# Optimization experiments

Hardware: AMD Instinct MI355X
Metric: run time of the kernel (lower is better)

The kernel has to match this reference:

```python
import jax, jax.numpy as jnp
import numpy as np

N = 50000
E = 800000
D = 128          # in_dim = hidden_dim = out_dim
H = 4            # heads
C = D // H       # per-head channels = 32
L = 3            # num_layers
SLOPE = 0.2
BN_EPS = 1e-5


def setup_inputs() -> dict:
    key = jax.random.key(0)
    ks = jax.random.split(key, 12)
    x = jax.random.normal(ks[0], (N, D), dtype=jnp.float32)
    ei = jax.random.randint(ks[1], (2, E), 0, N, dtype=jnp.int64)
    # remove accidental self loops (PyG removes then re-adds them)
    src, dst = ei[0], ei[1]
    src = jnp.where(src == dst, (src + 1) % N, src)
    edge_index = jnp.stack([src, dst])
    s = 1.0 / np.sqrt(D)
    Wl = jax.random.normal(ks[2], (L, D, D), dtype=jnp.float32) * s
    Wr = jax.random.normal(ks[3], (L, D, D), dtype=jnp.float32) * s
    att = jax.random.normal(ks[4], (L, H, C), dtype=jnp.float32) * (1.0 / np.sqrt(C))
    bias = jnp.zeros((L, D), dtype=jnp.float32)
    Wres = jax.random.normal(ks[5], (L, D, D), dtype=jnp.float32) * s
    gamma = jnp.ones((L, D), dtype=jnp.float32)
    beta = jnp.zeros((L, D), dtype=jnp.float32)
    W_out = jax.random.normal(ks[6], (D, D), dtype=jnp.float32) * s
    b_out = jnp.zeros((D,), dtype=jnp.float32)
    return {"x": x, "edge_index": edge_index, "Wl": Wl, "Wr": Wr, "att": att,
            "bias": bias, "Wres": Wres, "gamma": gamma, "beta": beta,
            "W_out": W_out, "b_out": b_out}


def _segment_softmax(scores, seg, num_segments):
    # scores: [E, H], seg: [E] dst ids
    m = jax.ops.segment_max(scores, seg, num_segments=num_segments)  # [N, H]
    ex = jnp.exp(scores - m[seg])
    denom = jax.ops.segment_sum(ex, seg, num_segments=num_segments)  # [N, H]
    return ex / denom[seg]


def _gatv2_layer(x, src, dst, Wl_, Wr_, att_, b_, Wres_):
    xl = (x @ Wl_).reshape(N, H, C)   # source-side transform
    xr = (x @ Wr_).reshape(N, H, C)   # target-side transform
    msg = xl[src]                      # [E, H, C]
    pre = jax.nn.leaky_relu(msg + xr[dst], SLOPE)
    e = jnp.einsum('ehc,hc->eh', pre, att_)          # [E, H]
    alpha = _segment_softmax(e, dst, N)              # [E, H]
    agg = jax.ops.segment_sum(alpha[..., None] * msg, dst, num_segments=N)
    return agg.reshape(N, D) + b_ + x @ Wres_


def _batch_norm(x, g, b):
    mu = jnp.mean(x, axis=0)
    var = jnp.mean(jnp.square(x - mu), axis=0)  # biased, as in torch BN
    return (x - mu) * jax.lax.rsqrt(var + BN_EPS) * g + b


def reference(x, edge_index, Wl, Wr, att, bias, Wres, gamma, beta, W_out, b_out):
    # add self loops once (same augmentation every layer)
    loops = jnp.arange(N, dtype=edge_index.dtype)
    src = jnp.concatenate([edge_index[0], loops])
    dst = jnp.concatenate([edge_index[1], loops])
    for i in range(L):
        x = _gatv2_layer(x, src, dst, Wl[i], Wr[i], att[i], bias[i], Wres[i])
        x = _batch_norm(x, gamma[i], beta[i])
        x = jax.nn.leaky_relu(x, SLOPE)
        # dropout = identity in eval
    return x @ W_out + b_out
```

## Files before the change

### kernel.cpp

```cpp
#include <hip/hip_runtime.h>
#include <hip/hip_bf16.h>

constexpr int N = 50000;
constexpr int E = 800000;
constexpr int D = 128;
constexpr int H = 4;
constexpr int C = 32;
constexpr int L = 3;
constexpr int E2 = E + N;
constexpr float SLOPE = 0.2f;
constexpr float BN_EPS = 1e-5f;
constexpr float LOG2E = 1.4426950408889634f;
constexpr int TILES = (N + 63) / 64;

typedef __attribute__((ext_vector_type(8))) short bf16x8_t;
typedef __attribute__((ext_vector_type(4))) float f32x4_t;
typedef __attribute__((ext_vector_type(2))) float v2f;

using hbf = __hip_bfloat16;

__device__ __forceinline__ float fast_exp2(float x) { return __builtin_amdgcn_exp2f(x); }

__device__ __forceinline__ short f2bf(float v) {
    hbf h = __float2bfloat16(v);
    return *reinterpret_cast<short*>(&h);
}
__device__ __forceinline__ v2f bfpair_to_v2(unsigned int u) {
    v2f r;
    r.x = __uint_as_float(u << 16);
    r.y = __uint_as_float(u & 0xffff0000u);
    return r;
}

__global__ void count_kernel(const int* __restrict__ ei, int* __restrict__ counts,
                             int* __restrict__ rank) {
    int i = blockIdx.x * blockDim.x + threadIdx.x;
    if (i >= E2) return;
    int dst = (i < E) ? ei[E + i] : (i - E);
    rank[i] = atomicAdd(&counts[dst], 1);
}

__global__ __launch_bounds__(512) void scan_block_kernel(const int* __restrict__ counts,
                                                         int* __restrict__ row_ptr,
                                                         int* __restrict__ blk_sums) {
    __shared__ int s[512];
    int t = threadIdx.x;
    int i = blockIdx.x * 512 + t;
    int v = (i < N) ? counts[i] : 0;
    s[t] = v;
    __syncthreads();
    for (int off = 1; off < 512; off <<= 1) {
        int add = (t >= off) ? s[t - off] : 0;
        __syncthreads();
        s[t] += add;
        __syncthreads();
    }
    if (i < N) row_ptr[i] = s[t] - v;
    if (t == 511) blk_sums[blockIdx.x] = s[511];
}

__global__ __launch_bounds__(128) void scan_sums_kernel(int* __restrict__ blk, int nb) {
    __shared__ int s[128];
    int t = threadIdx.x;
    int v = (t < nb) ? blk[t] : 0;
    s[t] = v;
    __syncthreads();
    for (int off = 1; off < 128; off <<= 1) {
        int add = (t >= off) ? s[t - off] : 0;
        __syncthreads();
        s[t] += add;
        __syncthreads();
    }
    if (t < nb) blk[t] = s[t] - v;
}

__global__ void scan_add_kernel(int* __restrict__ row_ptr, const int* __restrict__ blk) {
    int i = blockIdx.x * blockDim.x + threadIdx.x;
    if (i < N) row_ptr[i] += blk[i >> 9];
    if (i == 0) row_ptr[N] = E2;
}

__global__ void scatter_kernel(const int* __restrict__ ei, const int* __restrict__ row_ptr,
                               const int* __restrict__ rank, int* __restrict__ col_idx) {
    int i = blockIdx.x * blockDim.x + threadIdx.x;
    if (i >= E2) return;
    int src, dst;
    if (i < E) { src = ei[i]; dst = ei[E + i]; }
    else       { src = i - E; dst = i - E; }
    col_idx[row_ptr[dst] + rank[i]] = src;
}

__global__ __launch_bounds__(256) void pack_w_kernel(
        const float* __restrict__ Wl, const float* __restrict__ Wr,
        const float* __restrict__ Wres, const float* __restrict__ Wout,
        hbf* __restrict__ Wph) {
    int gid = blockIdx.x * 256 + threadIdx.x;
    int mat = gid >> 14;
    int d = gid & 16383;
    const float* W;
    if (mat < 3)      W = Wl + (size_t)mat * 16384;
    else if (mat < 6) W = Wr + (size_t)(mat - 3) * 16384;
    else if (mat < 9) W = Wres + (size_t)(mat - 6) * 16384;
    else              W = Wout;
    int j = d & 7, lane = (d >> 3) & 63, nb = (d >> 9) & 7, ks = d >> 12;
    int k = ks * 32 + ((lane >> 4) * 8) + j;
    int n = nb * 16 + (lane & 15);
    Wph[gid] = __float2bfloat16(W[k * D + n]);
}

__global__ __launch_bounds__(256) void gemm3_mfma_kernel(
        const float* x, const float* __restrict__ sums,
        const float* __restrict__ gamma, const float* __restrict__ beta,
        const hbf* __restrict__ Wph,
        int mL, int mR, int mS, const float* __restrict__ bias,
        hbf* __restrict__ xl, hbf* __restrict__ xr, float* y) {
    __shared__ hbf xsh[64][136];
    __shared__ hbf xsl[64][136];
    __shared__ float ssl[2][128];
    int t = threadIdx.x;
    int wave = t >> 6;
    int lane = t & 63;
    int nb0 = wave * 2;
    int row0 = blockIdx.x * 64;

    if (sums && t < 128) {
        float mean = sums[t] * (1.0f / N);
        float var = fmaxf(sums[D + t] * (1.0f / N) - mean * mean, 0.f);
        float sc = gamma[t] * rsqrtf(var + BN_EPS);
        ssl[0][t] = sc;
        ssl[1][t] = beta[t] - mean * sc;
    }

    const bf16x8_t* B = (const bf16x8_t*)Wph;
    bf16x8_t bL[4][2], bR[4][2], bS[4][2];
#pragma unroll
    for (int ks = 0; ks < 4; ++ks)
#pragma unroll
        for (int j = 0; j < 2; ++j) {
            int bo = (ks * 8 + nb0 + j) * 64 + lane;
            bL[ks][j] = B[mL * 2048 + bo];
            bR[ks][j] = B[mR * 2048 + bo];
            bS[ks][j] = B[mS * 2048 + bo];
        }
    __syncthreads();

    int cg = (t & 31) * 4;
    {
        float sc_[4] = {1.f, 1.f, 1.f, 1.f}, sh_[4] = {0.f, 0.f, 0.f, 0.f};
        if (sums) {
#pragma unroll
            for (int j = 0; j < 4; ++j) { sc_[j] = ssl[0][cg + j]; sh_[j] = ssl[1][cg + j]; }
        }
        const float4* x4 = (const float4*)(x + (size_t)row0 * D);
        for (int i = t; i < 64 * 32; i += 256) {
            int r = i >> 5;
            float4 v = make_float4(0.f, 0.f, 0.f, 0.f);
            if (row0 + r < N) {
                v = x4[i];
                if (sums) {
                    v.x = fmaf(v.x, sc_[0], sh_[0]); v.x = fmaxf(v.x, SLOPE * v.x);
                    v.y = fmaf(v.y, sc_[1], sh_[1]); v.y = fmaxf(v.y, SLOPE * v.y);
                    v.z = fmaf(v.z, sc_[2], sh_[2]); v.z = fmaxf(v.z, SLOPE * v.z);
                    v.w = fmaf(v.w, sc_[3], sh_[3]); v.w = fmaxf(v.w, SLOPE * v.w);
                }
            }
            short h0 = f2bf(v.x), h1 = f2bf(v.y), h2 = f2bf(v.z), h3 = f2bf(v.w);
            float r0 = v.x - __uint_as_float(((unsigned)(unsigned short)h0) << 16);
            float r1 = v.y - __uint_as_float(((unsigned)(unsigned short)h1) << 16);
            float r2 = v.z - __uint_as_float(((unsigned)(unsigned short)h2) << 16);
            float r3 = v.w - __uint_as_float(((unsigned)(unsigned short)h3) << 16);
            short l0 = f2bf(r0), l1 = f2bf(r1), l2 = f2bf(r2), l3 = f2bf(r3);
            uint2 hp, lp;
            hp.x = (unsigned)(unsigned short)h0 | ((unsigned)(unsigned short)h1 << 16);
            hp.y = (unsigned)(unsigned short)h2 | ((unsigned)(unsigned short)h3 << 16);
            lp.x = (unsigned)(unsigned short)l0 | ((unsigned)(unsigned short)l1 << 16);
            lp.y = (unsigned)(unsigned short)l2 | ((unsigned)(unsigned short)l3 << 16);
            *(uint2*)&xsh[r][cg] = hp;
            *(uint2*)&xsl[r][cg] = lp;
        }
    }
    __syncthreads();

    int col = lane & 15;
    int koff = (lane >> 4) * 8;
    for (int mm = 0; mm < 4; ++mm) {
        int mrow = mm * 16 + (lane & 15);
        f32x4_t aL[2], aR[2], aS[2];
#pragma unroll
        for (int j = 0; j < 2; ++j) {
            aL[j] = (f32x4_t)0.f; aR[j] = (f32x4_t)0.f; aS[j] = (f32x4_t)0.f;
        }
#pragma unroll
        for (int ks = 0; ks < 4; ++ks) {
            bf16x8_t ah = *(const bf16x8_t*)&xsh[mrow][ks * 32 + koff];
            bf16x8_t al = *(const bf16x8_t*)&xsl[mrow][ks * 32 + koff];
#pragma unroll
            for (int j = 0; j < 2; ++j) {
                aL[j] = __builtin_amdgcn_mfma_f32_16x16x32_bf16(ah, bL[ks][j], aL[j], 0, 0, 0);
                aL[j] = __builtin_amdgcn_mfma_f32_16x16x32_bf16(al, bL[ks][j], aL[j], 0, 0, 0);
                aR[j] = __builtin_amdgcn_mfma_f32_16x16x32_bf16(ah, bR[ks][j], aR[j], 0, 0, 0);
                aR[j] = __builtin_amdgcn_mfma_f32_16x16x32_bf16(al, bR[ks][j], aR[j], 0, 0, 0);
                aS[j] = __builtin_amdgcn_mfma_f32_16x16x32_bf16(ah, bS[ks][j], aS[j], 0, 0, 0);
                aS[j] = __builtin_amdgcn_mfma_f32_16x16x32_bf16(al, bS[ks][j], aS[j], 0, 0, 0);
            }
        }
        int rowq = row0 + mm * 16 + (lane >> 4) * 4;
#pragma unroll
        for (int j = 0; j < 2; ++j) {
            int n = (nb0 + j) * 16 + col;
            float bv = bias[n];
#pragma unroll
            for (int r = 0; r < 4; ++r) {
                int row = rowq + r;
                if (row < N) {
                    xl[(size_t)row * D + n] = __float2bfloat16(aL[j][r]);
                    xr[(size_t)row * D + n] = __float2bfloat16(aR[j][r]);
                    y[(size_t)row * D + n]  = aS[j][r] + bv;
                }
            }
        }
    }
}

__global__ __launch_bounds__(256) void gemm_out_mfma_kernel(
        const float* __restrict__ x, const float* __restrict__ sums,
        const float* __restrict__ gamma, const float* __restrict__ beta,
        const hbf* __restrict__ Wph, const float* __restrict__ b,
        float* __restrict__ out) {
    __shared__ hbf xsh[64][136];
    __shared__ hbf xsl[64][136];
    __shared__ float ssl[2][128];
    int t = threadIdx.x;
    int wave = t >> 6;
    int lane = t & 63;
    int nb0 = wave * 2;
    int row0 = blockIdx.x * 64;

    if (t < 128) {
        float mean = sums[t] * (1.0f / N);
        float var = fmaxf(sums[D + t] * (1.0f / N) - mean * mean, 0.f);
        float sc = gamma[t] * rsqrtf(var + BN_EPS);
        ssl[0][t] = sc;
        ssl[1][t] = beta[t] - mean * sc;
    }

    const bf16x8_t* B = (const bf16x8_t*)Wph + 9 * 2048;
    bf16x8_t bW[4][2];
#pragma unroll
    for (int ks = 0; ks < 4; ++ks)
#pragma unroll
        for (int j = 0; j < 2; ++j)
            bW[ks][j] = B[(ks * 8 + nb0 + j) * 64 + lane];
    __syncthreads();

    int cg = (t & 31) * 4;
    {
        float sc_[4], sh_[4];
#pragma unroll
        for (int j = 0; j < 4; ++j) { sc_[j] = ssl[0][cg + j]; sh_[j] = ssl[1][cg + j]; }
        const float4* x4 = (const float4*)(x + (size_t)row0 * D);
        for (int i = t; i < 64 * 32; i += 256) {
            int r = i >> 5;
            float4 v = make_float4(0.f, 0.f, 0.f, 0.f);
            if (row0 + r < N) {
                v = x4[i];
                v.x = fmaf(v.x, sc_[0], sh_[0]); v.x = fmaxf(v.x, SLOPE * v.x);
                v.y = fmaf(v.y, sc_[1], sh_[1]); v.y = fmaxf(v.y, SLOPE * v.y);
                v.z = fmaf(v.z, sc_[2], sh_[2]); v.z = fmaxf(v.z, SLOPE * v.z);
                v.w = fmaf(v.w, sc_[3], sh_[3]); v.w = fmaxf(v.w, SLOPE * v.w);
            }
            short h0 = f2bf(v.x), h1 = f2bf(v.y), h2 = f2bf(v.z), h3 = f2bf(v.w);
            float r0 = v.x - __uint_as_float(((unsigned)(unsigned short)h0) << 16);
            float r1 = v.y - __uint_as_float(((unsigned)(unsigned short)h1) << 16);
            float r2 = v.z - __uint_as_float(((unsigned)(unsigned short)h2) << 16);
            float r3 = v.w - __uint_as_float(((unsigned)(unsigned short)h3) << 16);
            short l0 = f2bf(r0), l1 = f2bf(r1), l2 = f2bf(r2), l3 = f2bf(r3);
            uint2 hp, lp;
            hp.x = (unsigned)(unsigned short)h0 | ((unsigned)(unsigned short)h1 << 16);
            hp.y = (unsigned)(unsigned short)h2 | ((unsigned)(unsigned short)h3 << 16);
            lp.x = (unsigned)(unsigned short)l0 | ((unsigned)(unsigned short)l1 << 16);
            lp.y = (unsigned)(unsigned short)l2 | ((unsigned)(unsigned short)l3 << 16);
            *(uint2*)&xsh[r][cg] = hp;
            *(uint2*)&xsl[r][cg] = lp;
        }
    }
    __syncthreads();

    int col = lane & 15;
    int koff = (lane >> 4) * 8;
    for (int mm = 0; mm < 4; ++mm) {
        int mrow = mm * 16 + (lane & 15);
        f32x4_t acc[2];
        acc[0] = (f32x4_t)0.f; acc[1] = (f32x4_t)0.f;
#pragma unroll
        for (int ks = 0; ks < 4; ++ks) {
            bf16x8_t ah = *(const bf16x8_t*)&xsh[mrow][ks * 32 + koff];
            bf16x8_t al = *(const bf16x8_t*)&xsl[mrow][ks * 32 + koff];
#pragma unroll
            for (int j = 0; j < 2; ++j) {
                acc[j] = __builtin_amdgcn_mfma_f32_16x16x32_bf16(ah, bW[ks][j], acc[j], 0, 0, 0);
                acc[j] = __builtin_amdgcn_mfma_f32_16x16x32_bf16(al, bW[ks][j], acc[j], 0, 0, 0);
            }
        }
        int rowq = row0 + mm * 16 + (lane >> 4) * 4;
#pragma unroll
        for (int j = 0; j < 2; ++j) {
            int n = (nb0 + j) * 16 + col;
            float bv = b[n];
#pragma unroll
            for (int r = 0; r < 4; ++r) {
                int row = rowq + r;
                if (row < N) out[(size_t)row * D + n] = acc[j][r] + bv;
            }
        }
    }
}

__global__ __launch_bounds__(256) void gat_kernel(
        const hbf* __restrict__ xl, const hbf* __restrict__ xr,
        float* y, const int* __restrict__ row_ptr,
        const int* __restrict__ col_idx, const float* __restrict__ att) {
    int wave = threadIdx.x >> 6;
    int lane = threadIdx.x & 63;
    int e    = (lane >> 4) & 1;
    int sub  = lane & 15;
    int v = blockIdx.x * 8 + wave * 2 + (lane >> 5);
    const uint4* xlp = (const uint4*)xl;
    const uint4* xrp = (const uint4*)xr;
    uint4 xru = xrp[(size_t)v * 16 + sub];
    v2f xr_a = bfpair_to_v2(xru.x);
    v2f xr_b = bfpair_to_v2(xru.y);
    v2f xr_c = bfpair_to_v2(xru.z);
    v2f xr_d = bfpair_to_v2(xru.w);
    const float4* attf = (const float4*)att;
    float4 a4lo = attf[sub * 2];
    float4 a4hi = attf[sub * 2 + 1];
    v2f a_a; a_a.x = a4lo.x * LOG2E; a_a.y = a4lo.y * LOG2E;
    v2f a_b; a_b.x = a4lo.z * LOG2E; a_b.y = a4lo.w * LOG2E;
    v2f a_c; a_c.x = a4hi.x * LOG2E; a_c.y = a4hi.y * LOG2E;
    v2f a_d; a_d.x = a4hi.z * LOG2E; a_d.y = a4hi.w * LOG2E;
    int beg = row_ptr[v], end = row_ptr[v + 1];
    int d = end - beg;
    int dmax = max(d, __shfl_xor(d, 32));
    float l = 0.f;
    v2f acc_a = {0.f, 0.f};
    v2f acc_b = {0.f, 0.f};
    v2f acc_c = {0.f, 0.f};
    v2f acc_d = {0.f, 0.f};

    uint4 u0[2], u1[2];
    int c0[2], c1[2];
    u0[0] = xlp[(size_t)col_idx[min(beg + 0 + e, end - 1)] * 16 + sub];
    u0[1] = xlp[(size_t)col_idx[min(beg + 2 + e, end - 1)] * 16 + sub];
    u1[0] = xlp[(size_t)col_idx[min(beg + 4 + e, end - 1)] * 16 + sub];
    u1[1] = xlp[(size_t)col_idx[min(beg + 6 + e, end - 1)] * 16 + sub];
    c0[0] = col_idx[min(beg + 8 + e, end - 1)];
    c0[1] = col_idx[min(beg + 10 + e, end - 1)];
    c1[0] = col_idx[min(beg + 12 + e, end - 1)];
    c1[1] = col_idx[min(beg + 14 + e, end - 1)];

    int off = 0;
    auto process4 = [&](uint4 (&buf)[2], int (&cid)[2]) {
        v2f xa0 = bfpair_to_v2(buf[0].x);
        v2f xb0 = bfpair_to_v2(buf[0].y);
        v2f xc0 = bfpair_to_v2(buf[0].z);
        v2f xd0 = bfpair_to_v2(buf[0].w);
        v2f xa1 = bfpair_to_v2(buf[1].x);
        v2f xb1 = bfpair_to_v2(buf[1].y);
        v2f xc1 = bfpair_to_v2(buf[1].z);
        v2f xd1 = bfpair_to_v2(buf[1].w);
        buf[0] = xlp[(size_t)cid[0] * 16 + sub];
        buf[1] = xlp[(size_t)cid[1] * 16 + sub];
        cid[0] = col_idx[min(beg + off + 16 + e, end - 1)];
        cid[1] = col_idx[min(beg + off + 18 + e, end - 1)];

        v2f pa = xa0 + xr_a, pb = xb0 + xr_b;
        v2f pc = xc0 + xr_c, pd = xd0 + xr_d;
        pa = __builtin_elementwise_max(pa, pa * SLOPE);
        pb = __builtin_elementwise_max(pb, pb * SLOPE);
        pc = __builtin_elementwise_max(pc, pc * SLOPE);
        pd = __builtin_elementwise_max(pd, pd * SLOPE);
        v2f t0 = pa * a_a;
        t0 = pb * a_b + t0;
        t0 = pc * a_c + t0;
        t0 = pd * a_d + t0;
        pa = xa1 + xr_a; pb = xb1 + xr_b;
        pc = xc1 + xr_c; pd = xd1 + xr_d;
        pa = __builtin_elementwise_max(pa, pa * SLOPE);
        pb = __builtin_elementwise_max(pb, pb * SLOPE);
        pc = __builtin_elementwise_max(pc, pc * SLOPE);
        pd = __builtin_elementwise_max(pd, pd * SLOPE);
        v2f t1 = pa * a_a;
        t1 = pb * a_b + t1;
        t1 = pc * a_c + t1;
        t1 = pd * a_d + t1;
        float s0 = t0.x + t0.y;
        float s1 = t1.x + t1.y;
        s0 += __shfl_xor(s0, 1);  s1 += __shfl_xor(s1, 1);
        s0 += __shfl_xor(s0, 2);  s1 += __shfl_xor(s1, 2);
        float w0 = fast_exp2(s0);
        float w1 = fast_exp2(s1);
        w0 = (off + e < d) ? w0 : 0.f;
        w1 = (off + 2 + e < d) ? w1 : 0.f;
        l += w0 + w1;
        acc_a = xa0 * w0 + acc_a;
        acc_b = xb0 * w0 + acc_b;
        acc_c = xc0 * w0 + acc_c;
        acc_d = xd0 * w0 + acc_d;
        acc_a = xa1 * w1 + acc_a;
        acc_b = xb1 * w1 + acc_b;
        acc_c = xc1 * w1 + acc_c;
        acc_d = xd1 * w1 + acc_d;
    };

    while (true) {
        process4(u0, c0);
        off += 4;
        if (off >= dmax) break;
        process4(u1, c1);
        off += 4;
        if (off >= dmax) break;
    }
    l += __shfl_xor(l, 16);
    acc_a.x += __shfl_xor(acc_a.x, 16); acc_a.y += __shfl_xor(acc_a.y, 16);
    acc_b.x += __shfl_xor(acc_b.x, 16); acc_b.y += __shfl_xor(acc_b.y, 16);
    acc_c.x += __shfl_xor(acc_c.x, 16); acc_c.y += __shfl_xor(acc_c.y, 16);
    acc_d.x += __shfl_xor(acc_d.x, 16); acc_d.y += __shfl_xor(acc_d.y, 16);
    if (e == 0) {
        float rl = 1.f / l;
        size_t o = (size_t)v * 32 + sub * 2;
        float4 y0 = ((const float4*)y)[o];
        float4 y1 = ((const float4*)y)[o + 1];
        y0.x = fmaf(acc_a.x, rl, y0.x);
        y0.y = fmaf(acc_a.y, rl, y0.y);
        y0.z = fmaf(acc_b.x, rl, y0.z);
        y0.w = fmaf(acc_b.y, rl, y0.w);
        y1.x = fmaf(acc_c.x, rl, y1.x);
        y1.y = fmaf(acc_c.y, rl, y1.y);
        y1.z = fmaf(acc_d.x, rl, y1.z);
        y1.w = fmaf(acc_d.y, rl, y1.w);
        ((float4*)y)[o] = y0;
        ((float4*)y)[o + 1] = y1;
    }
}

__global__ __launch_bounds__(256) void bn_stats_kernel(const float* __restrict__ y,
                                                       float* __restrict__ sums) {
    __shared__ float ls[256][4];
    __shared__ float ls2[256][4];
    int t = threadIdx.x;
    float4 s = make_float4(0.f, 0.f, 0.f, 0.f);
    float4 s2 = make_float4(0.f, 0.f, 0.f, 0.f);
    const float4* y4 = (const float4*)y;
    for (int i = blockIdx.x * 256 + t; i < N * D / 4; i += gridDim.x * 256) {
        float4 v = y4[i];
        s.x += v.x; s.y += v.y; s.z += v.z; s.w += v.w;
        s2.x = fmaf(v.x, v.x, s2.x); s2.y = fmaf(v.y, v.y, s2.y);
        s2.z = fmaf(v.z, v.z, s2.z); s2.w = fmaf(v.w, v.w, s2.w);
    }
    ls[t][0] = s.x;  ls[t][1] = s.y;  ls[t][2] = s.z;  ls[t][3] = s.w;
    ls2[t][0] = s2.x; ls2[t][1] = s2.y; ls2[t][2] = s2.z; ls2[t][3] = s2.w;
    __syncthreads();
    if (t < D) {
        int g = t >> 2, e = t & 3;
        float a = 0.f, b = 0.f;
#pragma unroll
        for (int j = 0; j < 8; ++j) {
            a += ls[g + 32 * j][e];
            b += ls2[g + 32 * j][e];
        }
        atomicAdd(&sums[t], a);
        atomicAdd(&sums[D + t], b);
    }
}

extern "C" void kernel_launch(void* const* d_in, const int* in_sizes, int n_in,
                              void* d_out, int out_size, void* d_ws, size_t ws_size,
                              hipStream_t stream) {
    const float* x_in  = (const float*)d_in[0];
    const int*   ei    = (const int*)d_in[1];
    const float* Wl    = (const float*)d_in[2];
    const float* Wr    = (const float*)d_in[3];
    const float* att   = (const float*)d_in[4];
    const float* bias  = (const float*)d_in[5];
    const float* Wres  = (const float*)d_in[6];
    const float* gamma = (const float*)d_in[7];
    const float* beta  = (const float*)d_in[8];
    const float* Wout  = (const float*)d_in[9];
    const float* bout  = (const float*)d_in[10];
    float* out = (float*)d_out;

    char* ws = (char*)d_ws;
    size_t off = 0;
    auto alloc = [&](size_t bytes) {
        void* p = ws + off;
        off = (off + bytes + 255) & ~(size_t)255;
        return p;
    };
    hbf*   xl       = (hbf*)alloc((size_t)N * D * sizeof(hbf));
    hbf*   xr       = (hbf*)alloc((size_t)N * D * sizeof(hbf));
    float* y        = (float*)alloc((size_t)N * D * sizeof(float));
    hbf*   Wph      = (hbf*)alloc((size_t)10 * D * D * sizeof(hbf));
    int*   row_ptr  = (int*)alloc((size_t)(N + 1) * sizeof(int));
    int*   col_idx  = (int*)alloc((size_t)E2 * sizeof(int));
    int*   counts   = (int*)alloc((size_t)N * sizeof(int));
    int*   rank     = (int*)alloc((size_t)E2 * sizeof(int));
    int*   blk_sums = (int*)alloc(128 * sizeof(int));
    float* sums     = (float*)alloc(3 * 2 * D * sizeof(float));

    const int NB = (N + 511) / 512;

    (void)hipMemsetAsync(counts, 0, (size_t)N * sizeof(int), stream);
    (void)hipMemsetAsync(sums, 0, 3 * 2 * D * sizeof(float), stream);
    count_kernel<<<(E2 + 255) / 256, 256, 0, stream>>>(ei, counts, rank);
    pack_w_kernel<<<10 * 16384 / 256, 256, 0, stream>>>(Wl, Wr, Wres, Wout, Wph);
    scan_block_kernel<<<NB, 512, 0, stream>>>(counts, row_ptr, blk_sums);
    scan_sums_kernel<<<1, 128, 0, stream>>>(blk_sums, NB);
    scan_add_kernel<<<(N + 255) / 256, 256, 0, stream>>>(row_ptr, blk_sums);
    scatter_kernel<<<(E2 + 255) / 256, 256, 0, stream>>>(ei, row_ptr, rank, col_idx);

    for (int i = 0; i < L; ++i) {
        const float* xin = (i == 0) ? x_in : y;
        const float* sm  = (i == 0) ? nullptr : sums + (size_t)(i - 1) * 2 * D;
        const float* ga  = (i == 0) ? nullptr : gamma + (size_t)(i - 1) * D;
        const float* be  = (i == 0) ? nullptr : beta + (size_t)(i - 1) * D;
        gemm3_mfma_kernel<<<TILES, 256, 0, stream>>>(xin, sm, ga, be, Wph,
                                                     i, 3 + i, 6 + i,
                                                     bias + (size_t)i * D, xl, xr, y);
        gat_kernel<<<N / 8, 256, 0, stream>>>(xl, xr, y, row_ptr, col_idx,
                                              att + (size_t)i * H * C);
        bn_stats_kernel<<<512, 256, 0, stream>>>(y, sums + (size_t)i * 2 * D);
    }

    gemm_out_mfma_kernel<<<TILES, 256, 0, stream>>>(y, sums + (size_t)2 * 2 * D,
                                                    gamma + (size_t)2 * D,
                                                    beta + (size_t)2 * D, Wph, bout, out);
}
```

Baseline: 404.3 us.

## Fuse batch-norm statistics into GAT aggregation kernel with partitioned atomics

Removes the separate bn_stats kernel. The GAT kernel now accumulates per-column sum and sum-of-squares for each block's 8 rows in shared memory, then atomically adds them into one of 32 partial buffers. The consumer GEMMs reduce the 32 partials when computing scale and shift. This avoids re-reading the 25 MB y array three times and saves launches, at the cost of 6250 blocks per layer doing atomics and an extra block-wide sync in the gather kernel.

After: 371.4 us (median of 2 runs). -8.1%, faster.

```diff
diff --git a/kernel.cpp b/kernel.cpp
--- a/kernel.cpp
+++ b/kernel.cpp
@@ -12,6 +12,7 @@
 constexpr float BN_EPS = 1e-5f;
 constexpr float LOG2E = 1.4426950408889634f;
 constexpr int TILES = (N + 63) / 64;
+constexpr int NPART = 32;
 
 typedef __attribute__((ext_vector_type(8))) short bf16x8_t;
 typedef __attribute__((ext_vector_type(4))) float f32x4_t;
@@ -124,8 +125,14 @@
     int row0 = blockIdx.x * 64;
 
     if (sums && t < 128) {
-        float mean = sums[t] * (1.0f / N);
-        float var = fmaxf(sums[D + t] * (1.0f / N) - mean * mean, 0.f);
+        float sm = 0.f, s2 = 0.f;
+#pragma unroll 8
+        for (int p = 0; p < NPART; ++p) {
+            sm += sums[p * 256 + t];
+            s2 += sums[p * 256 + 128 + t];
+        }
+        float mean = sm * (1.0f / N);
+        float var = fmaxf(s2 * (1.0f / N) - mean * mean, 0.f);
         float sc = gamma[t] * rsqrtf(var + BN_EPS);
         ssl[0][t] = sc;
         ssl[1][t] = beta[t] - mean * sc;
@@ -237,8 +244,14 @@
     int row0 = blockIdx.x * 64;
 
     if (t < 128) {
-        float mean = sums[t] * (1.0f / N);
-        float var = fmaxf(sums[D + t] * (1.0f / N) - mean * mean, 0.f);
+        float sm = 0.f, s2 = 0.f;
+#pragma unroll 8
+        for (int p = 0; p < NPART; ++p) {
+            sm += sums[p * 256 + t];
+            s2 += sums[p * 256 + 128 + t];
+        }
+        float mean = sm * (1.0f / N);
+        float var = fmaxf(s2 * (1.0f / N) - mean * mean, 0.f);
         float sc = gamma[t] * rsqrtf(var + BN_EPS);
         ssl[0][t] = sc;
         ssl[1][t] = beta[t] - mean * sc;
@@ -319,12 +332,16 @@
 __global__ __launch_bounds__(256) void gat_kernel(
         const hbf* __restrict__ xl, const hbf* __restrict__ xr,
         float* y, const int* __restrict__ row_ptr,
-        const int* __restrict__ col_idx, const float* __restrict__ att) {
+        const int* __restrict__ col_idx, const float* __restrict__ att,
+        float* __restrict__ bn_part) {
+    __shared__ float bs[8][132];
+    __shared__ float bs2[8][132];
     int wave = threadIdx.x >> 6;
     int lane = threadIdx.x & 63;
     int e    = (lane >> 4) & 1;
     int sub  = lane & 15;
-    int v = blockIdx.x * 8 + wave * 2 + (lane >> 5);
+    int half = lane >> 5;
+    int v = blockIdx.x * 8 + wave * 2 + half;
     const uint4* xlp = (const uint4*)xl;
     const uint4* xrp = (const uint4*)xr;
     uint4 xru = xrp[(size_t)v * 16 + sub];
@@ -441,36 +458,29 @@
         y1.w = fmaf(acc_d.y, rl, y1.w);
         ((float4*)y)[o] = y0;
         ((float4*)y)[o + 1] = y1;
-    }
-}
-
-__global__ __launch_bounds__(256) void bn_stats_kernel(const float* __restrict__ y,
-                                                       float* __restrict__ sums) {
-    __shared__ float ls[256][4];
-    __shared__ float ls2[256][4];
+        int rrow = wave * 2 + half;
+        int cb = sub * 8;
+        bs[rrow][cb + 0] = y0.x;  bs2[rrow][cb + 0] = y0.x * y0.x;
+        bs[rrow][cb + 1] = y0.y;  bs2[rrow][cb + 1] = y0.y * y0.y;
+        bs[rrow][cb + 2] = y0.z;  bs2[rrow][cb + 2] = y0.z * y0.z;
+        bs[rrow][cb + 3] = y0.w;  bs2[rrow][cb + 3] = y0.w * y0.w;
+        bs[rrow][cb + 4] = y1.x;  bs2[rrow][cb + 4] = y1.x * y1.x;
+        bs[rrow][cb + 5] = y1.y;  bs2[rrow][cb + 5] = y1.y * y1.y;
+        bs[rrow][cb + 6] = y1.z;  bs2[rrow][cb + 6] = y1.z * y1.z;
+        bs[rrow][cb + 7] = y1.w;  bs2[rrow][cb + 7] = y1.w * y1.w;
+    }
+    __syncthreads();
     int t = threadIdx.x;
-    float4 s = make_float4(0.f, 0.f, 0.f, 0.f);
-    float4 s2 = make_float4(0.f, 0.f, 0.f, 0.f);
-    const float4* y4 = (const float4*)y;
-    for (int i = blockIdx.x * 256 + t; i < N * D / 4; i += gridDim.x * 256) {
-        float4 v = y4[i];
-        s.x += v.x; s.y += v.y; s.z += v.z; s.w += v.w;
-        s2.x = fmaf(v.x, v.x, s2.x); s2.y = fmaf(v.y, v.y, s2.y);
-        s2.z = fmaf(v.z, v.z, s2.z); s2.w = fmaf(v.w, v.w, s2.w);
-    }
-    ls[t][0] = s.x;  ls[t][1] = s.y;  ls[t][2] = s.z;  ls[t][3] = s.w;
-    ls2[t][0] = s2.x; ls2[t][1] = s2.y; ls2[t][2] = s2.z; ls2[t][3] = s2.w;
-    __syncthreads();
-    if (t < D) {
-        int g = t >> 2, e = t & 3;
-        float a = 0.f, b = 0.f;
-#pragma unroll
-        for (int j = 0; j < 8; ++j) {
-            a += ls[g + 32 * j][e];
-            b += ls2[g + 32 * j][e];
-        }
-        atomicAdd(&sums[t], a);
-        atomicAdd(&sums[D + t], b);
+    if (t < 128) {
+        float a = 0.f, b2 = 0.f;
+#pragma unroll
+        for (int r = 0; r < 8; ++r) {
+            a  += bs[r][t];
+            b2 += bs2[r][t];
+        }
+        float* part = bn_part + (size_t)(blockIdx.x & (NPART - 1)) * 256;
+        atomicAdd(&part[t], a);
+        atomicAdd(&part[128 + t], b2);
     }
 }
 
@@ -506,12 +516,12 @@
     int*   counts   = (int*)alloc((size_t)N * sizeof(int));
     int*   rank     = (int*)alloc((size_t)E2 * sizeof(int));
     int*   blk_sums = (int*)alloc(128 * sizeof(int));
-    float* sums     = (float*)alloc(3 * 2 * D * sizeof(float));
+    float* sums     = (float*)alloc((size_t)3 * NPART * 256 * sizeof(float));
 
     const int NB = (N + 511) / 512;
 
     (void)hipMemsetAsync(counts, 0, (size_t)N * sizeof(int), stream);
-    (void)hipMemsetAsync(sums, 0, 3 * 2 * D * sizeof(float), stream);
+    (void)hipMemsetAsync(sums, 0, (size_t)3 * NPART * 256 * sizeof(float), stream);
     count_kernel<<<(E2 + 255) / 256, 256, 0, stream>>>(ei, counts, rank);
     pack_w_kernel<<<10 * 16384 / 256, 256, 0, stream>>>(Wl, Wr, Wres, Wout, Wph);
     scan_block_kernel<<<NB, 512, 0, stream>>>(counts, row_ptr, blk_sums);
@@ -521,18 +531,18 @@
 
     for (int i = 0; i < L; ++i) {
         const float* xin = (i == 0) ? x_in : y;
-        const float* sm  = (i == 0) ? nullptr : sums + (size_t)(i - 1) * 2 * D;
+        const float* sm  = (i == 0) ? nullptr : sums + (size_t)(i - 1) * NPART * 256;
         const float* ga  = (i == 0) ? nullptr : gamma + (size_t)(i - 1) * D;
         const float* be  = (i == 0) ? nullptr : beta + (size_t)(i - 1) * D;
         gemm3_mfma_kernel<<<TILES, 256, 0, stream>>>(xin, sm, ga, be, Wph,
                                                      i, 3 + i, 6 + i,
                                                      bias + (size_t)i * D, xl, xr, y);
         gat_kernel<<<N / 8, 256, 0, stream>>>(xl, xr, y, row_ptr, col_idx,
-                                              att + (size_t)i * H * C);
-        bn_stats_kernel<<<512, 256, 0, stream>>>(y, sums + (size_t)i * 2 * D);
-    }
-
-    gemm_out_mfma_kernel<<<TILES, 256, 0, stream>>>(y, sums + (size_t)2 * 2 * D,
+                                              att + (size_t)i * H * C,
+                                              sums + (size_t)i * NPART * 256);
+    }
+
+    gemm_out_mfma_kernel<<<TILES, 256, 0, stream>>>(y, sums + (size_t)2 * NPART * 256,
                                                     gamma + (size_t)2 * D,
                                                     beta + (size_t)2 * D, Wph, bout, out);
 }
```
